# Kernel tuning notes

Measured on AMD Instinct MI355X. Metric: run time of the kernel, lower is better.

The kernel has to match this reference:

```python
import jax, jax.numpy as jnp
import numpy as np

FP4_VALUES = jnp.array([0.0, 0.5, 1.0, 1.5, 2.0, 3.0, 4.0, 6.0,
                        -0.0, -0.5, -1.0, -1.5, -2.0, -3.0, -4.0, -6.0], dtype=jnp.float32)
ALPHA = 1.702   # swiglu alpha
LIMIT = 7.0     # swiglu clamp limit
TOP_K = 4       # experts per token
EPS = 1e-5      # rmsnorm eps


def dequant_mxfp4(blocks, scales):
    """blocks: [E, R, G, B] int (uint8 values), scales: [E, R, G] int (E8M0 biased exp).
    Returns decoded weights [E, R, G*2B] fp32. Low nibble -> even cols, high nibble -> odd."""
    lo = FP4_VALUES[blocks & 15]
    hi = FP4_VALUES[(blocks >> 4) & 15]
    vals = jnp.stack([lo, hi], axis=-1).reshape(blocks.shape[:-1] + (-1,))  # [E,R,G,2B]
    w = jnp.ldexp(vals, (scales - 127)[..., None])
    return w.reshape(blocks.shape[:-2] + (-1,))


def rmsnorm(x, w):
    return x * jax.lax.rsqrt(jnp.mean(x * x, axis=-1, keepdims=True) + EPS) * w


def setup_inputs():
    key = jax.random.key(0)
    ks = jax.random.split(key, 10)
    E, H, I, B, S = 32, 1024, 1024, 1, 1024
    GB = 16  # packed bytes per 32-element group
    return {
        "x": jax.random.normal(ks[0], (B, S, H), jnp.float32),
        "norm_w": jnp.ones((H,), jnp.float32),
        "gate_w": jax.random.normal(ks[1], (E, H), jnp.float32) * 0.05,
        "gate_b": jax.random.normal(ks[2], (E,), jnp.float32) * 0.01,
        "mlp1_bias": jax.random.normal(ks[3], (E, 2 * I), jnp.float32) * 0.02,
        "mlp2_bias": jax.random.normal(ks[4], (E, H), jnp.float32) * 0.02,
        "mlp1_blocks": jax.random.randint(ks[5], (E, 2 * I, H // 32, GB), 0, 256, jnp.int32),
        "mlp1_scales": jax.random.randint(ks[6], (E, 2 * I, H // 32), 118, 125, jnp.int32),
        "mlp2_blocks": jax.random.randint(ks[7], (E, H, I // 32, GB), 0, 256, jnp.int32),
        "mlp2_scales": jax.random.randint(ks[8], (E, H, I // 32), 118, 125, jnp.int32),
    }


def reference(x, norm_w, gate_w, gate_b, mlp1_bias, mlp2_bias,
              mlp1_blocks, mlp1_scales, mlp2_blocks, mlp2_scales):
    B, S, H = x.shape
    N = B * S
    E = gate_w.shape[0]

    t = rmsnorm(x, norm_w).reshape(N, H)
    logits = t @ gate_w.T + gate_b                      # [N, E]
    top_vals, top_idx = jax.lax.top_k(logits, TOP_K)     # sorted descending, like torch.topk
    top_w = jax.nn.softmax(top_vals, axis=-1)            # [N, K]
    # dense routing matrix: nonzero only at selected experts (indices unique per token)
    route = jnp.zeros((N, E), x.dtype).at[jnp.arange(N)[:, None], top_idx].add(top_w)

    w1 = dequant_mxfp4(mlp1_blocks, mlp1_scales)         # [E, 2I, H]
    w2 = dequant_mxfp4(mlp2_blocks, mlp2_scales)         # [E, H, I]

    h = jnp.einsum('nh,eih->nei', t, w1) + mlp1_bias[None]  # [N, E, 2I]
    x_glu = jnp.minimum(h[..., 0::2], LIMIT)
    x_lin = jnp.clip(h[..., 1::2], -LIMIT, LIMIT)
    a = x_glu * jax.nn.sigmoid(ALPHA * x_glu) * (x_lin + 1.0)   # [N, E, I]
    y = jnp.einsum('nei,ehi->neh', a, w2) + mlp2_bias[None]      # [N, E, H]
    out = jnp.einsum('neh,ne->nh', y, route)                     # weighted combine
    return x + out.reshape(B, S, H)
```

## Files before the change

kernel.cpp:

```cpp
#include <hip/hip_runtime.h>
#include <hip/hip_bf16.h>
#include <math.h>


#define NE 32
#define HD 1024
#define ID 1024
#define NTOK 1024
#define R1 2048

typedef __attribute__((ext_vector_type(8)))  short bf16x8;
typedef __attribute__((ext_vector_type(16))) float f32x16;

#define TB_OFF   0
#define A_OFF    2097152
#define YB_OFF   10485760
#define CNT_OFF  18874368
#define OFFS_OFF 18874624
#define TOKL_OFF 18874880
#define TIDX_OFF 19005952
#define TWT_OFF  19022336
#define POS_OFF  19038720

__device__ __forceinline__ unsigned f2bf(float f) {
    unsigned u = __float_as_uint(f);
    return (u + 0x7FFFu + ((u >> 16) & 1u)) >> 16;
}
__device__ __forceinline__ float bf2f(unsigned u) {
    return __uint_as_float(u << 16);
}

__device__ __forceinline__ bf16x8 dec8(int4 wv, unsigned dd) {
    unsigned u = __builtin_amdgcn_perm((unsigned)wv.y, (unsigned)wv.x, 0x00000400u);
    unsigned v = __builtin_amdgcn_perm((unsigned)wv.w, (unsigned)wv.z, 0x04000000u);
    unsigned packed = __builtin_amdgcn_perm(v, u, 0x07060100u);
    unsigned selE = packed & 0x07070707u;
    unsigned sE   = packed & 0x08080808u;
    unsigned ph   = packed >> 4;
    unsigned selO = ph & 0x07070707u;
    unsigned sO   = ph & 0x08080808u;
    const unsigned PH_hi = 0x40404040u, PH_lo = 0x3F3F3F14u;
    const unsigned PL_hi = 0xC0804000u, PL_lo = 0xC0800000u;
    unsigned hbE = __builtin_amdgcn_perm(PH_hi, PH_lo, selE) | (sE << 4);
    unsigned lbE = __builtin_amdgcn_perm(PL_hi, PL_lo, selE);
    unsigned hbO = __builtin_amdgcn_perm(PH_hi, PH_lo, selO) | (sO << 4);
    unsigned lbO = __builtin_amdgcn_perm(PL_hi, PL_lo, selO);
    unsigned mE0 = __builtin_amdgcn_perm(hbE, lbE, 0x05010400u);
    unsigned mE1 = __builtin_amdgcn_perm(hbE, lbE, 0x07030602u);
    unsigned mO0 = __builtin_amdgcn_perm(hbO, lbO, 0x05010400u);
    unsigned mO1 = __builtin_amdgcn_perm(hbO, lbO, 0x07030602u);
    unsigned r0 = __builtin_amdgcn_perm(mO0, mE0, 0x05040100u);
    unsigned r1 = __builtin_amdgcn_perm(mO0, mE0, 0x07060302u);
    unsigned r2 = __builtin_amdgcn_perm(mO1, mE1, 0x05040100u);
    unsigned r3 = __builtin_amdgcn_perm(mO1, mE1, 0x07060302u);
    unsigned o0, o1, o2, o3;
    asm("v_pk_add_u16 %0, %1, %2" : "=v"(o0) : "v"(r0), "v"(dd));
    asm("v_pk_add_u16 %0, %1, %2" : "=v"(o1) : "v"(r1), "v"(dd));
    asm("v_pk_add_u16 %0, %1, %2" : "=v"(o2) : "v"(r2), "v"(dd));
    asm("v_pk_add_u16 %0, %1, %2" : "=v"(o3) : "v"(r3), "v"(dd));
    uint4 o; o.x = o0; o.y = o1; o.z = o2; o.w = o3;
    union { uint4 u4; bf16x8 b; } cv; cv.u4 = o;
    return cv.b;
}

__device__ __forceinline__ void fence_lds() {
    asm volatile("s_waitcnt lgkmcnt(0)" ::: "memory");
    __builtin_amdgcn_sched_barrier(0);
    __builtin_amdgcn_s_barrier();
    __builtin_amdgcn_sched_barrier(0);
}

__global__ __launch_bounds__(256) void k_gate(
    const float* __restrict__ x, const float* __restrict__ norm_w,
    const float* __restrict__ gate_w, const float* __restrict__ gate_b,
    ushort* __restrict__ t_bf16, int* __restrict__ top_idx, float* __restrict__ top_wt,
    int* __restrict__ counts, int* __restrict__ tok_list, int* __restrict__ pos_of)
{
    int n = blockIdx.x;
    int tid = threadIdx.x;
    __shared__ float tl[HD];
    __shared__ float red[4];
    __shared__ float logits[NE];

    const float4* xv = (const float4*)(x + (size_t)n * HD);
    float4 v = xv[tid];
    float ss = v.x * v.x + v.y * v.y + v.z * v.z + v.w * v.w;
    #pragma unroll
    for (int off = 32; off; off >>= 1) ss += __shfl_down(ss, off);
    if ((tid & 63) == 0) red[tid >> 6] = ss;
    __syncthreads();
    float tot = red[0] + red[1] + red[2] + red[3];
    float rms = rsqrtf(tot * (1.0f / HD) + 1e-5f);

    float4 w = ((const float4*)norm_w)[tid];
    float4 tv;
    tv.x = v.x * rms * w.x; tv.y = v.y * rms * w.y;
    tv.z = v.z * rms * w.z; tv.w = v.w * rms * w.w;
    ushort4 tb;
    tb.x = (ushort)f2bf(tv.x); tb.y = (ushort)f2bf(tv.y);
    tb.z = (ushort)f2bf(tv.z); tb.w = (ushort)f2bf(tv.w);
    ((ushort4*)(t_bf16 + (size_t)n * HD))[tid] = tb;
    ((float4*)tl)[tid] = tv;
    __syncthreads();

    int wv = tid >> 6, lane = tid & 63;
    for (int j = 0; j < 8; j++) {
        int e = wv * 8 + j;
        const float* gw = gate_w + (size_t)e * HD;
        float p = 0.f;
        #pragma unroll
        for (int q = 0; q < 16; q++) { int kk = lane + q * 64; p += tl[kk] * gw[kk]; }
        #pragma unroll
        for (int off = 32; off; off >>= 1) p += __shfl_down(p, off);
        if (lane == 0) logits[e] = p + gate_b[e];
    }
    __syncthreads();

    if (tid == 0) {
        float vals[4]; int idx[4];
        unsigned used = 0;
        #pragma unroll
        for (int kk = 0; kk < 4; kk++) {
            float best = -1e30f; int bi = 0;
            for (int e2 = 0; e2 < NE; e2++) {
                if (used & (1u << e2)) continue;
                if (logits[e2] > best) { best = logits[e2]; bi = e2; }
            }
            used |= 1u << bi; vals[kk] = best; idx[kk] = bi;
        }
        float m = vals[0], s = 0.f, ex[4];
        #pragma unroll
        for (int kk = 0; kk < 4; kk++) { ex[kk] = __expf(vals[kk] - m); s += ex[kk]; }
        float inv = 1.0f / s;
        #pragma unroll
        for (int kk = 0; kk < 4; kk++) {
            top_idx[n * 4 + kk] = idx[kk];
            top_wt[n * 4 + kk] = ex[kk] * inv;
            int slot = atomicAdd(counts + idx[kk], 1);
            tok_list[idx[kk] * NTOK + slot] = n;
            pos_of[n * 4 + kk] = slot;
        }
    }
}

__global__ void k_prefix(const int* __restrict__ counts, int* __restrict__ offsets)
{
    if (threadIdx.x == 0) {
        int s = 0;
        for (int e = 0; e < NE; e++) { offsets[e] = s; s += counts[e]; }
        offsets[NE] = s;
    }
}

__global__ __launch_bounds__(256) void k_mlp1(
    const ushort* __restrict__ t_bf16, const int* __restrict__ blocks,
    const int* __restrict__ scales, const float* __restrict__ bias,
    const int* __restrict__ counts, const int* __restrict__ offsets,
    const int* __restrict__ tok_list, ushort* __restrict__ a)
{
    int e = blockIdx.y;
    int cnt = counts[e];
    int r0 = blockIdx.x * 128;
    int tid = threadIdx.x;
    int l = tid & 63;
    int lr = l & 31, kh = l >> 5;
    int base = offsets[e];

    __shared__ ushort tl[2][64][72];

    int row = r0 + (tid >> 6) * 32 + lr;
    const int4* wp = (const int4*)blocks + (size_t)(e * R1 + row) * 128 + kh;
    const int*  sp = scales + (size_t)(e * R1 + row) * 32;
    float bl = bias[e * R1 + row];
    int srow = tid & 63;
    int scol0 = (tid >> 6) * 8;
    int scol1 = scol0 + 32;

    for (int c0 = blockIdx.z * 64; c0 < cnt; c0 += 256) {
        int nt = min(64, cnt - c0);
        int nmt = (nt + 31) >> 5;
        const ushort* tp = t_bf16 + (size_t)tok_list[e * NTOK + c0 + min(srow, nt - 1)] * HD;

        uint4 t0a = *(const uint4*)(tp + scol0);
        uint4 t0b = *(const uint4*)(tp + scol1);
        int4 wbA[4], wbB[4]; int2 scA, scB;
        #pragma unroll
        for (int ks = 0; ks < 4; ks++) wbA[ks] = wp[2 * ks];
        scA = *(const int2*)sp;
        #pragma unroll
        for (int ks = 0; ks < 4; ks++) wbB[ks] = wp[8 + 2 * ks];
        scB = *(const int2*)(sp + 2);
        uint4 tra = *(const uint4*)(tp + 64 + scol0);
        uint4 trb = *(const uint4*)(tp + 64 + scol1);
        *(uint4*)&tl[0][srow][scol0] = t0a;
        *(uint4*)&tl[0][srow][scol1] = t0b;
        fence_lds();

        f32x16 acc[2] = {};

        #pragma unroll 1
        for (int kt2 = 0; kt2 < 16; kt2 += 2) {
            #pragma unroll
            for (int h = 0; h < 2; h++) {
                int kt = kt2 + h;
                int sA = h ? scB.x : scA.x;
                int sB = h ? scB.y : scA.y;
                unsigned dA16 = (unsigned)((sA - 127) << 7) & 0xFFFFu;
                unsigned dB16 = (unsigned)((sB - 127) << 7) & 0xFFFFu;
                unsigned dA = dA16 | (dA16 << 16), dB = dB16 | (dB16 << 16);
                bf16x8 wf0 = dec8(h ? wbB[0] : wbA[0], dA);
                bf16x8 wf1 = dec8(h ? wbB[1] : wbA[1], dA);
                bf16x8 wf2 = dec8(h ? wbB[2] : wbA[2], dB);
                bf16x8 wf3 = dec8(h ? wbB[3] : wbA[3], dB);
                if (kt < 15) {
                    *(uint4*)&tl[h ^ 1][srow][scol0] = tra;
                    *(uint4*)&tl[h ^ 1][srow][scol1] = trb;
                }
                if (kt < 14) {
                    const ushort* tpk = tp + (kt + 2) * 64;
                    tra = *(const uint4*)(tpk + scol0);
                    trb = *(const uint4*)(tpk + scol1);
                    int woff = (kt + 2) * 8;
                    if (h) {
                        #pragma unroll
                        for (int ks = 0; ks < 4; ks++) wbB[ks] = wp[woff + 2 * ks];
                        scB = *(const int2*)(sp + (kt + 2) * 2);
                    } else {
                        #pragma unroll
                        for (int ks = 0; ks < 4; ks++) wbA[ks] = wp[woff + 2 * ks];
                        scA = *(const int2*)(sp + (kt + 2) * 2);
                    }
                }
                #pragma unroll
                for (int mt = 0; mt < 2; mt++) {
                    if (mt < nmt) {
                        bf16x8 af0 = *(const bf16x8*)&tl[h][mt * 32 + lr][kh * 8];
                        acc[mt] = __builtin_amdgcn_mfma_f32_32x32x16_bf16(af0, wf0, acc[mt], 0, 0, 0);
                        bf16x8 af1 = *(const bf16x8*)&tl[h][mt * 32 + lr][16 + kh * 8];
                        acc[mt] = __builtin_amdgcn_mfma_f32_32x32x16_bf16(af1, wf1, acc[mt], 0, 0, 0);
                        bf16x8 af2 = *(const bf16x8*)&tl[h][mt * 32 + lr][32 + kh * 8];
                        acc[mt] = __builtin_amdgcn_mfma_f32_32x32x16_bf16(af2, wf2, acc[mt], 0, 0, 0);
                        bf16x8 af3 = *(const bf16x8*)&tl[h][mt * 32 + lr][48 + kh * 8];
                        acc[mt] = __builtin_amdgcn_mfma_f32_32x32x16_bf16(af3, wf3, acc[mt], 0, 0, 0);
                    }
                }
                fence_lds();
            }
        }

        #pragma unroll
        for (int mt = 0; mt < 2; mt++) {
            #pragma unroll
            for (int r = 0; r < 16; r++) {
                float hv = acc[mt][r] + bl;
                float other = __shfl_xor(hv, 1, 64);
                int m = (r & 3) + 8 * (r >> 2) + 4 * kh;
                int tokg = c0 + mt * 32 + m;
                if (!(l & 1) && tokg < cnt) {
                    float hg = fminf(hv, 7.0f);
                    float hx = fminf(fmaxf(other, -7.0f), 7.0f);
                    float sig = 1.0f / (1.0f + __expf(-1.702f * hg));
                    float av = hg * sig * (hx + 1.0f);
                    a[(size_t)(base + tokg) * ID + (row >> 1)] = (ushort)f2bf(av);
                }
            }
        }
    }
}

__global__ __launch_bounds__(256) void k_mlp2(
    const ushort* __restrict__ a, const int* __restrict__ blocks,
    const int* __restrict__ scales, const float* __restrict__ bias,
    const int* __restrict__ counts, const int* __restrict__ offsets,
    ushort* __restrict__ yb)
{
    int e = blockIdx.y;
    int cnt = counts[e];
    int r0 = blockIdx.x * 128;
    int tid = threadIdx.x;
    int l = tid & 63;
    int lr = l & 31, kh = l >> 5;
    int base = offsets[e];

    __shared__ ushort tl[2][64][72];

    int row = r0 + (tid >> 6) * 32 + lr;
    const int4* wp = (const int4*)blocks + (size_t)(e * HD + row) * 128 + kh;
    const int*  sp = scales + (size_t)(e * HD + row) * 32;
    float bl = bias[e * HD + row];
    int srow = tid & 63;
    int scol0 = (tid >> 6) * 8;
    int scol1 = scol0 + 32;

    for (int c0 = blockIdx.z * 64; c0 < cnt; c0 += 256) {
        int nt = min(64, cnt - c0);
        int nmt = (nt + 31) >> 5;
        const ushort* tp = a + (size_t)(base + c0 + min(srow, nt - 1)) * ID;

        uint4 t0a = *(const uint4*)(tp + scol0);
        uint4 t0b = *(const uint4*)(tp + scol1);
        int4 wbA[4], wbB[4]; int2 scA, scB;
        #pragma unroll
        for (int ks = 0; ks < 4; ks++) wbA[ks] = wp[2 * ks];
        scA = *(const int2*)sp;
        #pragma unroll
        for (int ks = 0; ks < 4; ks++) wbB[ks] = wp[8 + 2 * ks];
        scB = *(const int2*)(sp + 2);
        uint4 tra = *(const uint4*)(tp + 64 + scol0);
        uint4 trb = *(const uint4*)(tp + 64 + scol1);
        *(uint4*)&tl[0][srow][scol0] = t0a;
        *(uint4*)&tl[0][srow][scol1] = t0b;
        fence_lds();

        f32x16 acc[2] = {};

        #pragma unroll 1
        for (int kt2 = 0; kt2 < 16; kt2 += 2) {
            #pragma unroll
            for (int h = 0; h < 2; h++) {
                int kt = kt2 + h;
                int sA = h ? scB.x : scA.x;
                int sB = h ? scB.y : scA.y;
                unsigned dA16 = (unsigned)((sA - 127) << 7) & 0xFFFFu;
                unsigned dB16 = (unsigned)((sB - 127) << 7) & 0xFFFFu;
                unsigned dA = dA16 | (dA16 << 16), dB = dB16 | (dB16 << 16);
                bf16x8 wf0 = dec8(h ? wbB[0] : wbA[0], dA);
                bf16x8 wf1 = dec8(h ? wbB[1] : wbA[1], dA);
                bf16x8 wf2 = dec8(h ? wbB[2] : wbA[2], dB);
                bf16x8 wf3 = dec8(h ? wbB[3] : wbA[3], dB);
                if (kt < 15) {
                    *(uint4*)&tl[h ^ 1][srow][scol0] = tra;
                    *(uint4*)&tl[h ^ 1][srow][scol1] = trb;
                }
                if (kt < 14) {
                    const ushort* tpk = tp + (kt + 2) * 64;
                    tra = *(const uint4*)(tpk + scol0);
                    trb = *(const uint4*)(tpk + scol1);
                    int woff = (kt + 2) * 8;
                    if (h) {
                        #pragma unroll
                        for (int ks = 0; ks < 4; ks++) wbB[ks] = wp[woff + 2 * ks];
                        scB = *(const int2*)(sp + (kt + 2) * 2);
                    } else {
                        #pragma unroll
                        for (int ks = 0; ks < 4; ks++) wbA[ks] = wp[woff + 2 * ks];
                        scA = *(const int2*)(sp + (kt + 2) * 2);
                    }
                }
                #pragma unroll
                for (int mt = 0; mt < 2; mt++) {
                    if (mt < nmt) {
                        bf16x8 af0 = *(const bf16x8*)&tl[h][mt * 32 + lr][kh * 8];
                        acc[mt] = __builtin_amdgcn_mfma_f32_32x32x16_bf16(af0, wf0, acc[mt], 0, 0, 0);
                        bf16x8 af1 = *(const bf16x8*)&tl[h][mt * 32 + lr][16 + kh * 8];
                        acc[mt] = __builtin_amdgcn_mfma_f32_32x32x16_bf16(af1, wf1, acc[mt], 0, 0, 0);
                        bf16x8 af2 = *(const bf16x8*)&tl[h][mt * 32 + lr][32 + kh * 8];
                        acc[mt] = __builtin_amdgcn_mfma_f32_32x32x16_bf16(af2, wf2, acc[mt], 0, 0, 0);
                        bf16x8 af3 = *(const bf16x8*)&tl[h][mt * 32 + lr][48 + kh * 8];
                        acc[mt] = __builtin_amdgcn_mfma_f32_32x32x16_bf16(af3, wf3, acc[mt], 0, 0, 0);
                    }
                }
                fence_lds();
            }
        }

        #pragma unroll
        for (int mt = 0; mt < 2; mt++) {
            #pragma unroll
            for (int r = 0; r < 16; r++) {
                int m = (r & 3) + 8 * (r >> 2) + 4 * kh;
                int tokg = c0 + mt * 32 + m;
                if (tokg < cnt) {
                    float y = acc[mt][r] + bl;
                    yb[(size_t)(base + tokg) * HD + row] = (ushort)f2bf(y);
                }
            }
        }
    }
}

__global__ __launch_bounds__(256) void k_combine(
    const float* __restrict__ x, const ushort* __restrict__ yb,
    const int* __restrict__ top_idx, const float* __restrict__ top_wt,
    const int* __restrict__ pos_of, const int* __restrict__ offsets,
    float* __restrict__ out)
{
    int n = blockIdx.x, tid = threadIdx.x;
    float4 xv = ((const float4*)(x + (size_t)n * HD))[tid];
    float r0 = xv.x, r1 = xv.y, r2 = xv.z, r3 = xv.w;
    #pragma unroll
    for (int k = 0; k < 4; k++) {
        int e = top_idx[n * 4 + k];
        float wt = top_wt[n * 4 + k];
        int slot = offsets[e] + pos_of[n * 4 + k];
        ushort4 yv = ((const ushort4*)(yb + (size_t)slot * HD))[tid];
        r0 += wt * bf2f(yv.x); r1 += wt * bf2f(yv.y);
        r2 += wt * bf2f(yv.z); r3 += wt * bf2f(yv.w);
    }
    float4 ov; ov.x = r0; ov.y = r1; ov.z = r2; ov.w = r3;
    ((float4*)(out + (size_t)n * HD))[tid] = ov;
}

extern "C" void kernel_launch(void* const* d_in, const int* in_sizes, int n_in,
                              void* d_out, int out_size, void* d_ws, size_t ws_size,
                              hipStream_t stream)
{
    const float* x           = (const float*)d_in[0];
    const float* norm_w      = (const float*)d_in[1];
    const float* gate_w      = (const float*)d_in[2];
    const float* gate_b      = (const float*)d_in[3];
    const float* mlp1_bias   = (const float*)d_in[4];
    const float* mlp2_bias   = (const float*)d_in[5];
    const int*   mlp1_blocks = (const int*)d_in[6];
    const int*   mlp1_scales = (const int*)d_in[7];
    const int*   mlp2_blocks = (const int*)d_in[8];
    const int*   mlp2_scales = (const int*)d_in[9];
    float* out = (float*)d_out;

    char* ws = (char*)d_ws;
    ushort* t_bf16  = (ushort*)(ws + TB_OFF);
    ushort* a       = (ushort*)(ws + A_OFF);
    ushort* yb      = (ushort*)(ws + YB_OFF);
    int*   counts   = (int*)(ws + CNT_OFF);
    int*   offsets  = (int*)(ws + OFFS_OFF);
    int*   tok_list = (int*)(ws + TOKL_OFF);
    int*   top_idx  = (int*)(ws + TIDX_OFF);
    float* top_wt   = (float*)(ws + TWT_OFF);
    int*   pos_of   = (int*)(ws + POS_OFF);

    hipMemsetAsync(counts, 0, NE * sizeof(int), stream);
    k_gate<<<NTOK, 256, 0, stream>>>(x, norm_w, gate_w, gate_b, t_bf16, top_idx, top_wt,
                                     counts, tok_list, pos_of);
    k_prefix<<<1, 64, 0, stream>>>(counts, offsets);
    k_mlp1<<<dim3(16, NE, 4), 256, 0, stream>>>(t_bf16, mlp1_blocks, mlp1_scales, mlp1_bias,
                                                counts, offsets, tok_list, a);
    k_mlp2<<<dim3(8, NE, 4), 256, 0, stream>>>(a, mlp2_blocks, mlp2_scales, mlp2_bias,
                                               counts, offsets, yb);
    k_combine<<<NTOK, 256, 0, stream>>>(x, yb, top_idx, top_wt, pos_of, offsets, out);
}
```

Baseline: 191.5 us.

## Stream MXFP4 weight tiles into LDS via global_load_lds with swizzled layout

Both expert GEMM kernels now copy the packed FP4 weight tiles straight from global memory into double-buffered, XOR-swizzled LDS using global_load_lds, instead of holding them in registers. The token tile load is rearranged so each thread copies 32 contiguous bytes. The grid's z-split drops from 4 to 2, and launch bounds now request 3 blocks per CU. The aim is to cut register pressure, improve coalescing and overlap weight fetch with compute, but the waits now cover both vmcnt and lgkmcnt at every step, and the extra 32 KB of LDS per block may limit occupancy.

```diff
diff --git a/kernel.cpp b/kernel.cpp
--- a/kernel.cpp
+++ b/kernel.cpp
@@ -63,8 +63,14 @@
     return cv.b;
 }
 
-__device__ __forceinline__ void fence_lds() {
-    asm volatile("s_waitcnt lgkmcnt(0)" ::: "memory");
+__device__ __forceinline__ void gll16(const void* g, void* l) {
+    __builtin_amdgcn_global_load_lds(
+        (const __attribute__((address_space(1))) unsigned int*)g,
+        (__attribute__((address_space(3))) unsigned int*)l, 16, 0, 0);
+}
+
+__device__ __forceinline__ void fence_all() {
+    asm volatile("s_waitcnt vmcnt(0) lgkmcnt(0)" ::: "memory");
     __builtin_amdgcn_sched_barrier(0);
     __builtin_amdgcn_s_barrier();
     __builtin_amdgcn_sched_barrier(0);
@@ -152,7 +158,7 @@
     }
 }
 
-__global__ __launch_bounds__(256) void k_mlp1(
+__global__ __launch_bounds__(256, 3) void k_mlp1(
     const ushort* __restrict__ t_bf16, const int* __restrict__ blocks,
     const int* __restrict__ scales, const float* __restrict__ bias,
     const int* __restrict__ counts, const int* __restrict__ offsets,
@@ -164,87 +170,83 @@
     int tid = threadIdx.x;
     int l = tid & 63;
     int lr = l & 31, kh = l >> 5;
+    int w = tid >> 6;
+    int wu = __builtin_amdgcn_readfirstlane(w);
     int base = offsets[e];
 
     __shared__ ushort tl[2][64][72];
-
-    int row = r0 + (tid >> 6) * 32 + lr;
-    const int4* wp = (const int4*)blocks + (size_t)(e * R1 + row) * 128 + kh;
-    const int*  sp = scales + (size_t)(e * R1 + row) * 32;
+    __shared__ char   wlds[2][16384];
+
+    int row = r0 + w * 32 + lr;
+    const int* sp = scales + (size_t)(e * R1 + row) * 32;
     float bl = bias[e * R1 + row];
-    int srow = tid & 63;
-    int scol0 = (tid >> 6) * 8;
-    int scol1 = scol0 + 32;
-
-    for (int c0 = blockIdx.z * 64; c0 < cnt; c0 += 256) {
+    int swzr = (lr & 7) << 4;
+
+    int scol = ((l & 7) * 16) ^ ((l >> 3) << 4);
+    const char* pw[4];
+    #pragma unroll
+    for (int j = 0; j < 4; j++)
+        pw[j] = (const char*)blocks +
+                (size_t)(e * R1 + r0 + wu * 8 + (l >> 3) + j * 32) * 2048 + scol;
+
+    int trow = tid >> 2;
+    int tseg = (tid & 3) * 16;
+
+    for (int c0 = blockIdx.z * 64; c0 < cnt; c0 += 128) {
         int nt = min(64, cnt - c0);
         int nmt = (nt + 31) >> 5;
-        const ushort* tp = t_bf16 + (size_t)tok_list[e * NTOK + c0 + min(srow, nt - 1)] * HD;
-
-        uint4 t0a = *(const uint4*)(tp + scol0);
-        uint4 t0b = *(const uint4*)(tp + scol1);
-        int4 wbA[4], wbB[4]; int2 scA, scB;
-        #pragma unroll
-        for (int ks = 0; ks < 4; ks++) wbA[ks] = wp[2 * ks];
-        scA = *(const int2*)sp;
-        #pragma unroll
-        for (int ks = 0; ks < 4; ks++) wbB[ks] = wp[8 + 2 * ks];
-        scB = *(const int2*)(sp + 2);
-        uint4 tra = *(const uint4*)(tp + 64 + scol0);
-        uint4 trb = *(const uint4*)(tp + 64 + scol1);
-        *(uint4*)&tl[0][srow][scol0] = t0a;
-        *(uint4*)&tl[0][srow][scol1] = t0b;
-        fence_lds();
+        int tok_c = trow < nt ? trow : nt - 1;
+        const ushort* tp = t_bf16 + (size_t)tok_list[e * NTOK + c0 + tok_c] * HD + tseg;
+
+        #pragma unroll
+        for (int j = 0; j < 4; j++)
+            gll16(pw[j], &wlds[0][((j << 2) + wu) << 10]);
+        int2 sc = *(const int2*)sp;
+        uint4 trA = *(const uint4*)tp;
+        uint4 trB = *(const uint4*)(tp + 8);
+        *(uint4*)&tl[0][trow][tseg] = trA;
+        *(uint4*)&tl[0][trow][tseg + 8] = trB;
+        fence_all();
 
         f32x16 acc[2] = {};
+        int2 scn = sc;
 
         #pragma unroll 1
         for (int kt2 = 0; kt2 < 16; kt2 += 2) {
             #pragma unroll
             for (int h = 0; h < 2; h++) {
                 int kt = kt2 + h;
-                int sA = h ? scB.x : scA.x;
-                int sB = h ? scB.y : scA.y;
-                unsigned dA16 = (unsigned)((sA - 127) << 7) & 0xFFFFu;
-                unsigned dB16 = (unsigned)((sB - 127) << 7) & 0xFFFFu;
-                unsigned dA = dA16 | (dA16 << 16), dB = dB16 | (dB16 << 16);
-                bf16x8 wf0 = dec8(h ? wbB[0] : wbA[0], dA);
-                bf16x8 wf1 = dec8(h ? wbB[1] : wbA[1], dA);
-                bf16x8 wf2 = dec8(h ? wbB[2] : wbA[2], dB);
-                bf16x8 wf3 = dec8(h ? wbB[3] : wbA[3], dB);
-                if (kt < 15) {
-                    *(uint4*)&tl[h ^ 1][srow][scol0] = tra;
-                    *(uint4*)&tl[h ^ 1][srow][scol1] = trb;
-                }
-                if (kt < 14) {
-                    const ushort* tpk = tp + (kt + 2) * 64;
-                    tra = *(const uint4*)(tpk + scol0);
-                    trb = *(const uint4*)(tpk + scol1);
-                    int woff = (kt + 2) * 8;
-                    if (h) {
-                        #pragma unroll
-                        for (int ks = 0; ks < 4; ks++) wbB[ks] = wp[woff + 2 * ks];
-                        scB = *(const int2*)(sp + (kt + 2) * 2);
-                    } else {
-                        #pragma unroll
-                        for (int ks = 0; ks < 4; ks++) wbA[ks] = wp[woff + 2 * ks];
-                        scA = *(const int2*)(sp + (kt + 2) * 2);
+                bool pf = kt < 15;
+                if (pf) {
+                    #pragma unroll
+                    for (int j = 0; j < 4; j++)
+                        gll16(pw[j] + (kt + 1) * 128, &wlds[h ^ 1][((j << 2) + wu) << 10]);
+                    scn = *(const int2*)(sp + (kt + 1) * 2);
+                    trA = *(const uint4*)(tp + (kt + 1) * 64);
+                    trB = *(const uint4*)(tp + (kt + 1) * 64 + 8);
+                }
+                #pragma unroll
+                for (int ks = 0; ks < 4; ks++) {
+                    int s = ks < 2 ? sc.x : sc.y;
+                    unsigned dd16 = (unsigned)((s - 127) << 7) & 0xFFFFu;
+                    unsigned dd = dd16 | (dd16 << 16);
+                    int4 wv = *(const int4*)&wlds[h][(w * 32 + lr) * 128 +
+                                                     ((ks * 32 + kh * 16) ^ swzr)];
+                    bf16x8 wf = dec8(wv, dd);
+                    #pragma unroll
+                    for (int mt = 0; mt < 2; mt++) {
+                        if (mt < nmt) {
+                            bf16x8 af = *(const bf16x8*)&tl[h][mt * 32 + lr][ks * 16 + kh * 8];
+                            acc[mt] = __builtin_amdgcn_mfma_f32_32x32x16_bf16(af, wf, acc[mt], 0, 0, 0);
+                        }
                     }
                 }
-                #pragma unroll
-                for (int mt = 0; mt < 2; mt++) {
-                    if (mt < nmt) {
-                        bf16x8 af0 = *(const bf16x8*)&tl[h][mt * 32 + lr][kh * 8];
-                        acc[mt] = __builtin_amdgcn_mfma_f32_32x32x16_bf16(af0, wf0, acc[mt], 0, 0, 0);
-                        bf16x8 af1 = *(const bf16x8*)&tl[h][mt * 32 + lr][16 + kh * 8];
-                        acc[mt] = __builtin_amdgcn_mfma_f32_32x32x16_bf16(af1, wf1, acc[mt], 0, 0, 0);
-                        bf16x8 af2 = *(const bf16x8*)&tl[h][mt * 32 + lr][32 + kh * 8];
-                        acc[mt] = __builtin_amdgcn_mfma_f32_32x32x16_bf16(af2, wf2, acc[mt], 0, 0, 0);
-                        bf16x8 af3 = *(const bf16x8*)&tl[h][mt * 32 + lr][48 + kh * 8];
-                        acc[mt] = __builtin_amdgcn_mfma_f32_32x32x16_bf16(af3, wf3, acc[mt], 0, 0, 0);
-                    }
-                }
-                fence_lds();
+                if (pf) {
+                    *(uint4*)&tl[h ^ 1][trow][tseg] = trA;
+                    *(uint4*)&tl[h ^ 1][trow][tseg + 8] = trB;
+                }
+                fence_all();
+                sc = scn;
             }
         }
 
@@ -268,7 +270,7 @@
     }
 }
 
-__global__ __launch_bounds__(256) void k_mlp2(
+__global__ __launch_bounds__(256, 3) void k_mlp2(
     const ushort* __restrict__ a, const int* __restrict__ blocks,
     const int* __restrict__ scales, const float* __restrict__ bias,
     const int* __restrict__ counts, const int* __restrict__ offsets,
@@ -280,87 +282,83 @@
     int tid = threadIdx.x;
     int l = tid & 63;
     int lr = l & 31, kh = l >> 5;
+    int w = tid >> 6;
+    int wu = __builtin_amdgcn_readfirstlane(w);
     int base = offsets[e];
 
     __shared__ ushort tl[2][64][72];
-
-    int row = r0 + (tid >> 6) * 32 + lr;
-    const int4* wp = (const int4*)blocks + (size_t)(e * HD + row) * 128 + kh;
-    const int*  sp = scales + (size_t)(e * HD + row) * 32;
+    __shared__ char   wlds[2][16384];
+
+    int row = r0 + w * 32 + lr;
+    const int* sp = scales + (size_t)(e * HD + row) * 32;
     float bl = bias[e * HD + row];
-    int srow = tid & 63;
-    int scol0 = (tid >> 6) * 8;
-    int scol1 = scol0 + 32;
-
-    for (int c0 = blockIdx.z * 64; c0 < cnt; c0 += 256) {
+    int swzr = (lr & 7) << 4;
+
+    int scol = ((l & 7) * 16) ^ ((l >> 3) << 4);
+    const char* pw[4];
+    #pragma unroll
+    for (int j = 0; j < 4; j++)
+        pw[j] = (const char*)blocks +
+                (size_t)(e * HD + r0 + wu * 8 + (l >> 3) + j * 32) * 2048 + scol;
+
+    int trow = tid >> 2;
+    int tseg = (tid & 3) * 16;
+
+    for (int c0 = blockIdx.z * 64; c0 < cnt; c0 += 128) {
         int nt = min(64, cnt - c0);
         int nmt = (nt + 31) >> 5;
-        const ushort* tp = a + (size_t)(base + c0 + min(srow, nt - 1)) * ID;
-
-        uint4 t0a = *(const uint4*)(tp + scol0);
-        uint4 t0b = *(const uint4*)(tp + scol1);
-        int4 wbA[4], wbB[4]; int2 scA, scB;
-        #pragma unroll
-        for (int ks = 0; ks < 4; ks++) wbA[ks] = wp[2 * ks];
-        scA = *(const int2*)sp;
-        #pragma unroll
-        for (int ks = 0; ks < 4; ks++) wbB[ks] = wp[8 + 2 * ks];
-        scB = *(const int2*)(sp + 2);
-        uint4 tra = *(const uint4*)(tp + 64 + scol0);
-        uint4 trb = *(const uint4*)(tp + 64 + scol1);
-        *(uint4*)&tl[0][srow][scol0] = t0a;
-        *(uint4*)&tl[0][srow][scol1] = t0b;
-        fence_lds();
+        int tok_c = trow < nt ? trow : nt - 1;
+        const ushort* tp = a + (size_t)(base + c0 + tok_c) * ID + tseg;
+
+        #pragma unroll
+        for (int j = 0; j < 4; j++)
+            gll16(pw[j], &wlds[0][((j << 2) + wu) << 10]);
+        int2 sc = *(const int2*)sp;
+        uint4 trA = *(const uint4*)tp;
+        uint4 trB = *(const uint4*)(tp + 8);
+        *(uint4*)&tl[0][trow][tseg] = trA;
+        *(uint4*)&tl[0][trow][tseg + 8] = trB;
+        fence_all();
 
         f32x16 acc[2] = {};
+        int2 scn = sc;
 
         #pragma unroll 1
         for (int kt2 = 0; kt2 < 16; kt2 += 2) {
             #pragma unroll
             for (int h = 0; h < 2; h++) {
                 int kt = kt2 + h;
-                int sA = h ? scB.x : scA.x;
-                int sB = h ? scB.y : scA.y;
-                unsigned dA16 = (unsigned)((sA - 127) << 7) & 0xFFFFu;
-                unsigned dB16 = (unsigned)((sB - 127) << 7) & 0xFFFFu;
-                unsigned dA = dA16 | (dA16 << 16), dB = dB16 | (dB16 << 16);
-                bf16x8 wf0 = dec8(h ? wbB[0] : wbA[0], dA);
-                bf16x8 wf1 = dec8(h ? wbB[1] : wbA[1], dA);
-                bf16x8 wf2 = dec8(h ? wbB[2] : wbA[2], dB);
-                bf16x8 wf3 = dec8(h ? wbB[3] : wbA[3], dB);
-                if (kt < 15) {
-                    *(uint4*)&tl[h ^ 1][srow][scol0] = tra;
-                    *(uint4*)&tl[h ^ 1][srow][scol1] = trb;
-                }
-                if (kt < 14) {
-                    const ushort* tpk = tp + (kt + 2) * 64;
-                    tra = *(const uint4*)(tpk + scol0);
-                    trb = *(const uint4*)(tpk + scol1);
-                    int woff = (kt + 2) * 8;
-                    if (h) {
-                        #pragma unroll
-                        for (int ks = 0; ks < 4; ks++) wbB[ks] = wp[woff + 2 * ks];
-                        scB = *(const int2*)(sp + (kt + 2) * 2);
-                    } else {
-                        #pragma unroll
-                        for (int ks = 0; ks < 4; ks++) wbA[ks] = wp[woff + 2 * ks];
-                        scA = *(const int2*)(sp + (kt + 2) * 2);
+                bool pf = kt < 15;
+                if (pf) {
+                    #pragma unroll
+                    for (int j = 0; j < 4; j++)
+                        gll16(pw[j] + (kt + 1) * 128, &wlds[h ^ 1][((j << 2) + wu) << 10]);
+                    scn = *(const int2*)(sp + (kt + 1) * 2);
+                    trA = *(const uint4*)(tp + (kt + 1) * 64);
+                    trB = *(const uint4*)(tp + (kt + 1) * 64 + 8);
+                }
+                #pragma unroll
+                for (int ks = 0; ks < 4; ks++) {
+                    int s = ks < 2 ? sc.x : sc.y;
+                    unsigned dd16 = (unsigned)((s - 127) << 7) & 0xFFFFu;
+                    unsigned dd = dd16 | (dd16 << 16);
+                    int4 wv = *(const int4*)&wlds[h][(w * 32 + lr) * 128 +
+                                                     ((ks * 32 + kh * 16) ^ swzr)];
+                    bf16x8 wf = dec8(wv, dd);
+                    #pragma unroll
+                    for (int mt = 0; mt < 2; mt++) {
+                        if (mt < nmt) {
+                            bf16x8 af = *(const bf16x8*)&tl[h][mt * 32 + lr][ks * 16 + kh * 8];
+                            acc[mt] = __builtin_amdgcn_mfma_f32_32x32x16_bf16(af, wf, acc[mt], 0, 0, 0);
+                        }
                     }
                 }
-                #pragma unroll
-                for (int mt = 0; mt < 2; mt++) {
-                    if (mt < nmt) {
-                        bf16x8 af0 = *(const bf16x8*)&tl[h][mt * 32 + lr][kh * 8];
-                        acc[mt] = __builtin_amdgcn_mfma_f32_32x32x16_bf16(af0, wf0, acc[mt], 0, 0, 0);
-                        bf16x8 af1 = *(const bf16x8*)&tl[h][mt * 32 + lr][16 + kh * 8];
-                        acc[mt] = __builtin_amdgcn_mfma_f32_32x32x16_bf16(af1, wf1, acc[mt], 0, 0, 0);
-                        bf16x8 af2 = *(const bf16x8*)&tl[h][mt * 32 + lr][32 + kh * 8];
-                        acc[mt] = __builtin_amdgcn_mfma_f32_32x32x16_bf16(af2, wf2, acc[mt], 0, 0, 0);
-                        bf16x8 af3 = *(const bf16x8*)&tl[h][mt * 32 + lr][48 + kh * 8];
-                        acc[mt] = __builtin_amdgcn_mfma_f32_32x32x16_bf16(af3, wf3, acc[mt], 0, 0, 0);
-                    }
-                }
-                fence_lds();
+                if (pf) {
+                    *(uint4*)&tl[h ^ 1][trow][tseg] = trA;
+                    *(uint4*)&tl[h ^ 1][trow][tseg + 8] = trB;
+                }
+                fence_all();
+                sc = scn;
             }
         }
 
@@ -432,9 +430,9 @@
     k_gate<<<NTOK, 256, 0, stream>>>(x, norm_w, gate_w, gate_b, t_bf16, top_idx, top_wt,
                                      counts, tok_list, pos_of);
     k_prefix<<<1, 64, 0, stream>>>(counts, offsets);
-    k_mlp1<<<dim3(16, NE, 4), 256, 0, stream>>>(t_bf16, mlp1_blocks, mlp1_scales, mlp1_bias,
+    k_mlp1<<<dim3(16, NE, 2), 256, 0, stream>>>(t_bf16, mlp1_blocks, mlp1_scales, mlp1_bias,
                                                 counts, offsets, tok_list, a);
-    k_mlp2<<<dim3(8, NE, 4), 256, 0, stream>>>(a, mlp2_blocks, mlp2_scales, mlp2_bias,
+    k_mlp2<<<dim3(8, NE, 2), 256, 0, stream>>>(a, mlp2_blocks, mlp2_scales, mlp2_bias,
                                                counts, offsets, yb);
     k_combine<<<NTOK, 256, 0, stream>>>(x, yb, top_idx, top_wt, pos_of, offsets, out);
 }
```

Result: slower. 212.1 us (+10.7%).
